# Kernel tuning notes

Measured on AMD Instinct MI355X. Metric: run time of the kernel, lower is better.

Reference implementation:

```python
import jax, jax.numpy as jnp
import numpy as np

N_NODES = 100000
N_EDGES = 1600000
DIMS = [64, 64, 64, 32]  # [n_feat] + hid


def setup_inputs() -> dict:
    key = jax.random.key(0)
    ks = jax.random.split(key, 2 + 2 * (len(DIMS) - 1))
    x = jax.random.normal(ks[0], (N_NODES, DIMS[0]), dtype=jnp.float32)
    edge_index = jax.random.randint(ks[1], (2, N_EDGES), 0, N_NODES, dtype=jnp.int64)
    inp = {"x": x, "edge_index": edge_index}
    for i in range(len(DIMS) - 1):
        fan_in, fan_out = DIMS[i], DIMS[i + 1]
        scale = 1.0 / np.sqrt(fan_in)
        inp[f"W{i+1}"] = jax.random.normal(ks[2 + 2 * i], (fan_in, fan_out), dtype=jnp.float32) * scale
        inp[f"b{i+1}"] = jax.random.normal(ks[3 + 2 * i], (fan_out,), dtype=jnp.float32) * scale
    return inp


def _gcn_conv(x, W, b, src, dst, dis):
    # h = X W ; out[i] = sum_{j->i} norm_ij * h[j] + dis[i]^2 * h[i] + b
    h = x @ W
    norm = dis[src] * dis[dst]                      # [E]
    agg = jax.ops.segment_sum(h[src] * norm[:, None], dst, num_segments=x.shape[0])
    agg = agg + h * (dis * dis)[:, None]            # self-loop contribution
    return agg + b


def reference(x, edge_index, W1, b1, W2, b2, W3, b3):
    src, dst = edge_index[0], edge_index[1]
    n = x.shape[0]
    # degree with self-loops (edge weight 1), symmetric normalization
    deg = jax.ops.segment_sum(jnp.ones(src.shape[0], x.dtype), dst, num_segments=n) + 1.0
    dis = jax.lax.rsqrt(deg)
    h = jax.nn.relu(_gcn_conv(x, W1, b1, src, dst, dis))   # dropout is identity in eval
    h = jax.nn.relu(_gcn_conv(h, W2, b2, src, dst, dis))
    return _gcn_conv(h, W3, b3, src, dst, dis)
```

## Files before the change

kernel.cpp:

```cpp
#include <hip/hip_runtime.h>


typedef __attribute__((ext_vector_type(8))) _Float16 half8;
typedef __attribute__((ext_vector_type(4))) _Float16 half4;

static inline int cdiv(int a, int b) { return (a + b - 1) / b; }

#define ACHUNK 8192
#define MAXNBK 512

__global__ void k_bucket_hist(const int* __restrict__ dst, int* __restrict__ counts_t,
                              int NBK, int NBA, int E) {
    __shared__ int cnt[MAXNBK];
    int t = threadIdx.x, b = blockIdx.x;
    for (int i = t; i < NBK; i += 256) cnt[i] = 0;
    __syncthreads();
    int e0 = b * ACHUNK;
#pragma unroll 8
    for (int j = 0; j < ACHUNK / 256; ++j) {
        int e = e0 + j * 256 + t;
        if (e < E) atomicAdd(&cnt[dst[e] >> 8], 1);
    }
    __syncthreads();
    for (int i = t; i < NBK; i += 256) counts_t[i * NBA + b] = cnt[i];
}

#define SCAN_T 256
#define SCAN_V 4
#define SCAN_CHUNK 1024

__global__ void k_scan_partial(const int* __restrict__ a, int* __restrict__ bsum, int n) {
    __shared__ int red[SCAN_T];
    int t = threadIdx.x, b = blockIdx.x;
    int base = b * SCAN_CHUNK + t * SCAN_V;
    int s = 0;
#pragma unroll
    for (int j = 0; j < SCAN_V; ++j) { int i = base + j; if (i < n) s += a[i]; }
    red[t] = s;
    __syncthreads();
    for (int off = SCAN_T / 2; off > 0; off >>= 1) {
        if (t < off) red[t] += red[t + off];
        __syncthreads();
    }
    if (t == 0) bsum[b] = red[0];
}

__global__ void k_scan_final(const int* __restrict__ a, const int* __restrict__ bsum,
                             int* __restrict__ out, int nb, int n) {
    __shared__ int sb[256];
    __shared__ int sh[SCAN_T];
    int t = threadIdx.x, bk = blockIdx.x;
    sb[t] = (t < nb) ? bsum[t] : 0;
    __syncthreads();
    for (int off = 1; off < 256; off <<= 1) {
        int u = (t >= off) ? sb[t - off] : 0;
        __syncthreads();
        sb[t] += u;
        __syncthreads();
    }
    int bbase = (bk == 0) ? 0 : sb[bk - 1];
    int base = bk * SCAN_CHUNK + t * SCAN_V;
    int v[SCAN_V];
    int s = 0;
#pragma unroll
    for (int j = 0; j < SCAN_V; ++j) {
        int i = base + j;
        v[j] = (i < n) ? a[i] : 0;
        s += v[j];
    }
    sh[t] = s;
    __syncthreads();
    for (int off = 1; off < SCAN_T; off <<= 1) {
        int u = (t >= off) ? sh[t - off] : 0;
        __syncthreads();
        sh[t] += u;
        __syncthreads();
    }
    int run = sh[t] - s + bbase;
#pragma unroll
    for (int j = 0; j < SCAN_V; ++j) {
        int i = base + j;
        if (i < n) { out[i] = run; run += v[j]; }
    }
}

__global__ void k_bucket_scatter(const int* __restrict__ src, const int* __restrict__ dst,
                                 const int* __restrict__ offsets, unsigned* __restrict__ bucketed,
                                 int NBK, int NBA, int E) {
    __shared__ int curs[MAXNBK];
    int t = threadIdx.x, b = blockIdx.x;
    for (int i = t; i < NBK; i += 256) curs[i] = offsets[i * NBA + b];
    __syncthreads();
    int e0 = b * ACHUNK;
#pragma unroll 8
    for (int j = 0; j < ACHUNK / 256; ++j) {
        int e = e0 + j * 256 + t;
        if (e < E) {
            int d = dst[e];
            int pos = atomicAdd(&curs[d >> 8], 1);
            bucketed[pos] = (unsigned)src[e] | ((unsigned)(d & 255) << 24);
        }
    }
}

__global__ void k_bucket_build(const unsigned* __restrict__ bucketed,
                               const int* __restrict__ offsets,
                               int* __restrict__ csr_src, int* __restrict__ row_start,
                               float* __restrict__ dis, int NBK, int NBA, int N, int E) {
    __shared__ int cnt[256];
    __shared__ int sc[256];
    int t = threadIdx.x, k = blockIdx.x;
    int base = offsets[k * NBA];
    int end = (k + 1 < NBK) ? offsets[(k + 1) * NBA] : E;
    cnt[t] = 0;
    __syncthreads();
    for (int i = base + t; i < end; i += 256)
        atomicAdd(&cnt[bucketed[i] >> 24], 1);
    __syncthreads();
    int c = cnt[t];
    sc[t] = c;
    __syncthreads();
    for (int off = 1; off < 256; off <<= 1) {
        int u = (t >= off) ? sc[t - off] : 0;
        __syncthreads();
        sc[t] += u;
        __syncthreads();
    }
    int excl = sc[t] - c;
    int node = k * 256 + t;
    if (node < N) {
        row_start[node] = base + excl;
        dis[node] = rsqrtf(1.0f + (float)c);
    }
    if (k == 0 && t == 0) row_start[N] = E;
    cnt[t] = base + excl;
    __syncthreads();
    for (int i = base + t; i < end; i += 256) {
        unsigned w = bucketed[i];
        int pos = atomicAdd(&cnt[w >> 24], 1);
        csr_src[pos] = (int)(w & 0xFFFFFFu);
    }
}

template <int K, int M>
__global__ void k_gemm_f(const float* __restrict__ X, const float* __restrict__ W,
                         const float* __restrict__ dis, _Float16* __restrict__ H, int n) {
    constexpr int TPR = M / 8;
    constexpr int ROWS = 256 / TPR;
    constexpr int KP = K + 1;
    __shared__ float Ws[K * M];
    __shared__ float Xs[ROWS * KP];
    int tid = threadIdx.x;
    for (int idx = tid; idx < K * M / 4; idx += 256)
        ((float4*)Ws)[idx] = ((const float4*)W)[idx];
    int row0 = blockIdx.x * ROWS;
    for (int idx = tid; idx < ROWS * (K / 4); idx += 256) {
        int r = idx / (K / 4), kq = idx % (K / 4);
        int row = row0 + r;
        float4 vv = (row < n) ? ((const float4*)X)[(size_t)row * (K / 4) + kq]
                              : make_float4(0.f, 0.f, 0.f, 0.f);
        Xs[r * KP + kq * 4 + 0] = vv.x;
        Xs[r * KP + kq * 4 + 1] = vv.y;
        Xs[r * KP + kq * 4 + 2] = vv.z;
        Xs[r * KP + kq * 4 + 3] = vv.w;
    }
    __syncthreads();
    int r = tid / TPR, c0 = (tid % TPR) * 8;
    int row = row0 + r;
    if (row >= n) return;
    float4 a0 = make_float4(0.f, 0.f, 0.f, 0.f);
    float4 a1 = make_float4(0.f, 0.f, 0.f, 0.f);
#pragma unroll
    for (int k = 0; k < K; ++k) {
        float xv = Xs[r * KP + k];
        float4 w0 = ((const float4*)Ws)[(k * M + c0) / 4];
        float4 w1 = ((const float4*)Ws)[(k * M + c0) / 4 + 1];
        a0.x = fmaf(xv, w0.x, a0.x);
        a0.y = fmaf(xv, w0.y, a0.y);
        a0.z = fmaf(xv, w0.z, a0.z);
        a0.w = fmaf(xv, w0.w, a0.w);
        a1.x = fmaf(xv, w1.x, a1.x);
        a1.y = fmaf(xv, w1.y, a1.y);
        a1.z = fmaf(xv, w1.z, a1.z);
        a1.w = fmaf(xv, w1.w, a1.w);
    }
    float dn = dis[row];
    half8 hv;
    hv[0] = (_Float16)(a0.x * dn);
    hv[1] = (_Float16)(a0.y * dn);
    hv[2] = (_Float16)(a0.z * dn);
    hv[3] = (_Float16)(a0.w * dn);
    hv[4] = (_Float16)(a1.x * dn);
    hv[5] = (_Float16)(a1.y * dn);
    hv[6] = (_Float16)(a1.z * dn);
    hv[7] = (_Float16)(a1.w * dn);
    ((half8*)H)[(size_t)row * (M / 8) + c0 / 8] = hv;
}

template <int MOUT>
__global__ __launch_bounds__(256, 8)
void k_fused_agg_gemm(const _Float16* __restrict__ h, const float* __restrict__ dis,
                      const int* __restrict__ row_start, const int* __restrict__ csr_src,
                      const float* __restrict__ bagg, const float* __restrict__ W,
                      _Float16* __restrict__ H, int n) {
    constexpr int K = 64, KP = K + 1;
    __shared__ __align__(16) _Float16 Ws[K * MOUT];
    __shared__ float Xs[32 * KP];
    int tid = threadIdx.x;
    for (int idx = tid; idx < K * MOUT / 4; idx += 256) {
        float4 wv = ((const float4*)W)[idx];
        half4 h4;
        h4[0] = (_Float16)wv.x;
        h4[1] = (_Float16)wv.y;
        h4[2] = (_Float16)wv.z;
        h4[3] = (_Float16)wv.w;
        ((half4*)Ws)[idx] = h4;
    }

    int wave = tid >> 6, lane = tid & 63;
    int sub = lane >> 3, fl = lane & 7;
    int node0 = blockIdx.x * 32;
    int node = node0 + wave * 8 + sub;
    if (node < n) {
        const half8* h8 = (const half8*)h;
        float acc[8];
#pragma unroll
        for (int j = 0; j < 8; ++j) acc[j] = 0.f;
        int e = row_start[node], e1 = row_start[node + 1];
        for (; e + 7 < e1; e += 8) {
            int s0 = csr_src[e], s1 = csr_src[e + 1];
            int s2 = csr_src[e + 2], s3 = csr_src[e + 3];
            int s4 = csr_src[e + 4], s5 = csr_src[e + 5];
            int s6 = csr_src[e + 6], s7 = csr_src[e + 7];
            half8 v0 = h8[(size_t)s0 * 8 + fl];
            half8 v1 = h8[(size_t)s1 * 8 + fl];
            half8 v2 = h8[(size_t)s2 * 8 + fl];
            half8 v3 = h8[(size_t)s3 * 8 + fl];
            half8 v4 = h8[(size_t)s4 * 8 + fl];
            half8 v5 = h8[(size_t)s5 * 8 + fl];
            half8 v6 = h8[(size_t)s6 * 8 + fl];
            half8 v7 = h8[(size_t)s7 * 8 + fl];
#pragma unroll
            for (int j = 0; j < 8; ++j)
                acc[j] += (((float)v0[j] + (float)v1[j]) + ((float)v2[j] + (float)v3[j])) +
                          (((float)v4[j] + (float)v5[j]) + ((float)v6[j] + (float)v7[j]));
        }
        for (; e + 3 < e1; e += 4) {
            int s0 = csr_src[e], s1 = csr_src[e + 1];
            int s2 = csr_src[e + 2], s3 = csr_src[e + 3];
            half8 v0 = h8[(size_t)s0 * 8 + fl];
            half8 v1 = h8[(size_t)s1 * 8 + fl];
            half8 v2 = h8[(size_t)s2 * 8 + fl];
            half8 v3 = h8[(size_t)s3 * 8 + fl];
#pragma unroll
            for (int j = 0; j < 8; ++j)
                acc[j] += ((float)v0[j] + (float)v1[j]) + ((float)v2[j] + (float)v3[j]);
        }
        for (; e < e1; ++e) {
            int s0 = csr_src[e];
            half8 v0 = h8[(size_t)s0 * 8 + fl];
#pragma unroll
            for (int j = 0; j < 8; ++j) acc[j] += (float)v0[j];
        }
        float dn = dis[node];
        half8 hv = h8[(size_t)node * 8 + fl];
        float4 b0 = ((const float4*)bagg)[fl * 2];
        float4 b1 = ((const float4*)bagg)[fl * 2 + 1];
        int rrow = wave * 8 + sub;
        float* xp = &Xs[rrow * KP + fl * 8];
        xp[0] = fmaxf((acc[0] + (float)hv[0]) * dn + b0.x, 0.f);
        xp[1] = fmaxf((acc[1] + (float)hv[1]) * dn + b0.y, 0.f);
        xp[2] = fmaxf((acc[2] + (float)hv[2]) * dn + b0.z, 0.f);
        xp[3] = fmaxf((acc[3] + (float)hv[3]) * dn + b0.w, 0.f);
        xp[4] = fmaxf((acc[4] + (float)hv[4]) * dn + b1.x, 0.f);
        xp[5] = fmaxf((acc[5] + (float)hv[5]) * dn + b1.y, 0.f);
        xp[6] = fmaxf((acc[6] + (float)hv[6]) * dn + b1.z, 0.f);
        xp[7] = fmaxf((acc[7] + (float)hv[7]) * dn + b1.w, 0.f);
    }
    __syncthreads();

    constexpr int TPR = MOUT / 8;
    int r = tid / TPR, c0 = (tid % TPR) * 8;
    int row = node0 + r;
    if (r >= 32 || row >= n) return;
    float4 a0 = make_float4(0.f, 0.f, 0.f, 0.f);
    float4 a1 = make_float4(0.f, 0.f, 0.f, 0.f);
#pragma unroll
    for (int k = 0; k < K; ++k) {
        float xv = Xs[r * KP + k];
        half8 w = ((const half8*)Ws)[(k * MOUT + c0) / 8];
        a0.x = fmaf(xv, (float)w[0], a0.x);
        a0.y = fmaf(xv, (float)w[1], a0.y);
        a0.z = fmaf(xv, (float)w[2], a0.z);
        a0.w = fmaf(xv, (float)w[3], a0.w);
        a1.x = fmaf(xv, (float)w[4], a1.x);
        a1.y = fmaf(xv, (float)w[5], a1.y);
        a1.z = fmaf(xv, (float)w[6], a1.z);
        a1.w = fmaf(xv, (float)w[7], a1.w);
    }
    float dn = dis[row];
    half8 hv;
    hv[0] = (_Float16)(a0.x * dn);
    hv[1] = (_Float16)(a0.y * dn);
    hv[2] = (_Float16)(a0.z * dn);
    hv[3] = (_Float16)(a0.w * dn);
    hv[4] = (_Float16)(a1.x * dn);
    hv[5] = (_Float16)(a1.y * dn);
    hv[6] = (_Float16)(a1.z * dn);
    hv[7] = (_Float16)(a1.w * dn);
    ((half8*)H)[(size_t)row * (MOUT / 8) + c0 / 8] = hv;
}

__global__ __launch_bounds__(256, 8)
void k_aggregate32(const _Float16* __restrict__ h, const float* __restrict__ dis,
                   const int* __restrict__ row_start, const int* __restrict__ csr_src,
                   const float* __restrict__ b, float* __restrict__ out, int n) {
    constexpr int LPN = 4, NPW = 16;
    int gtid = blockIdx.x * blockDim.x + threadIdx.x;
    int wave = gtid >> 6;
    int lane = threadIdx.x & 63;
    int sub = lane / LPN, fl = lane % LPN;
    int node = wave * NPW + sub;
    if (node >= n) return;
    const half8* h8 = (const half8*)h;
    float acc[8];
#pragma unroll
    for (int j = 0; j < 8; ++j) acc[j] = 0.f;
    int e = row_start[node], e1 = row_start[node + 1];
    for (; e + 7 < e1; e += 8) {
        int s0 = csr_src[e], s1 = csr_src[e + 1];
        int s2 = csr_src[e + 2], s3 = csr_src[e + 3];
        int s4 = csr_src[e + 4], s5 = csr_src[e + 5];
        int s6 = csr_src[e + 6], s7 = csr_src[e + 7];
        half8 v0 = h8[(size_t)s0 * LPN + fl];
        half8 v1 = h8[(size_t)s1 * LPN + fl];
        half8 v2 = h8[(size_t)s2 * LPN + fl];
        half8 v3 = h8[(size_t)s3 * LPN + fl];
        half8 v4 = h8[(size_t)s4 * LPN + fl];
        half8 v5 = h8[(size_t)s5 * LPN + fl];
        half8 v6 = h8[(size_t)s6 * LPN + fl];
        half8 v7 = h8[(size_t)s7 * LPN + fl];
#pragma unroll
        for (int j = 0; j < 8; ++j)
            acc[j] += (((float)v0[j] + (float)v1[j]) + ((float)v2[j] + (float)v3[j])) +
                      (((float)v4[j] + (float)v5[j]) + ((float)v6[j] + (float)v7[j]));
    }
    for (; e + 3 < e1; e += 4) {
        int s0 = csr_src[e], s1 = csr_src[e + 1];
        int s2 = csr_src[e + 2], s3 = csr_src[e + 3];
        half8 v0 = h8[(size_t)s0 * LPN + fl];
        half8 v1 = h8[(size_t)s1 * LPN + fl];
        half8 v2 = h8[(size_t)s2 * LPN + fl];
        half8 v3 = h8[(size_t)s3 * LPN + fl];
#pragma unroll
        for (int j = 0; j < 8; ++j)
            acc[j] += ((float)v0[j] + (float)v1[j]) + ((float)v2[j] + (float)v3[j]);
    }
    for (; e < e1; ++e) {
        int s0 = csr_src[e];
        half8 v0 = h8[(size_t)s0 * LPN + fl];
#pragma unroll
        for (int j = 0; j < 8; ++j) acc[j] += (float)v0[j];
    }
    float dn = dis[node];
    half8 hv = h8[(size_t)node * LPN + fl];
    float4 b0 = ((const float4*)b)[fl * 2];
    float4 b1 = ((const float4*)b)[fl * 2 + 1];
    float4* op = (float4*)(out + ((size_t)node * LPN + fl) * 8);
    op[0] = make_float4((acc[0] + (float)hv[0]) * dn + b0.x,
                        (acc[1] + (float)hv[1]) * dn + b0.y,
                        (acc[2] + (float)hv[2]) * dn + b0.z,
                        (acc[3] + (float)hv[3]) * dn + b0.w);
    op[1] = make_float4((acc[4] + (float)hv[4]) * dn + b1.x,
                        (acc[5] + (float)hv[5]) * dn + b1.y,
                        (acc[6] + (float)hv[6]) * dn + b1.z,
                        (acc[7] + (float)hv[7]) * dn + b1.w);
}

extern "C" void kernel_launch(void* const* d_in, const int* in_sizes, int n_in,
                              void* d_out, int out_size, void* d_ws, size_t ws_size,
                              hipStream_t stream) {
    const float* x   = (const float*)d_in[0];
    const int*   ei  = (const int*)d_in[1];
    const float* W1  = (const float*)d_in[2];
    const float* b1  = (const float*)d_in[3];
    const float* W2  = (const float*)d_in[4];
    const float* b2  = (const float*)d_in[5];
    const float* W3  = (const float*)d_in[6];
    const float* b3  = (const float*)d_in[7];
    float* out = (float*)d_out;

    const int N = in_sizes[0] / 64;
    const int E = in_sizes[1] / 2;
    const int* src = ei;
    const int* dst = ei + E;

    const int NBK = cdiv(N, 256);
    const int NBA = cdiv(E, ACHUNK);
    const int nmat = NBK * NBA;

    const size_t Np = (size_t)((N + 63) / 64) * 64;
    char* p = (char*)d_ws;
    int*      counts_t = (int*)p;      p += (size_t)nmat * sizeof(int);
    int*      offsets  = (int*)p;      p += (size_t)nmat * sizeof(int);
    int*      bsum     = (int*)p;      p += 1024 * sizeof(int);
    int*      row_start= (int*)p;      p += (Np + 64) * sizeof(int);
    float*    dis      = (float*)p;    p += Np * sizeof(float);
    unsigned* bucketed = (unsigned*)p; p += (size_t)E * sizeof(unsigned);
    int*      csr_src  = (int*)p;      p += (size_t)E * sizeof(int);
    _Float16* bufA     = (_Float16*)p; p += Np * 64 * sizeof(_Float16);
    _Float16* bufB     = (_Float16*)p; p += Np * 64 * sizeof(_Float16);
    (void)ws_size;

    const int B = 256;
    const int nb = cdiv(nmat, SCAN_CHUNK);

    k_bucket_hist<<<NBA, B, 0, stream>>>(dst, counts_t, NBK, NBA, E);
    k_scan_partial<<<nb, B, 0, stream>>>(counts_t, bsum, nmat);
    k_scan_final<<<nb, B, 0, stream>>>(counts_t, bsum, offsets, nb, nmat);
    k_bucket_scatter<<<NBA, B, 0, stream>>>(src, dst, offsets, bucketed, NBK, NBA, E);
    k_bucket_build<<<NBK, B, 0, stream>>>(bucketed, offsets, csr_src, row_start, dis,
                                          NBK, NBA, N, E);

    k_gemm_f<64, 64><<<cdiv(N, 32), B, 0, stream>>>(x, W1, dis, bufA, N);
    k_fused_agg_gemm<64><<<cdiv(N, 32), B, 0, stream>>>(
        bufA, dis, row_start, csr_src, b1, W2, bufB, N);
    k_fused_agg_gemm<32><<<cdiv(N, 32), B, 0, stream>>>(
        bufB, dis, row_start, csr_src, b2, W3, bufA, N);
    k_aggregate32<<<cdiv(cdiv(N, 16) * 64, B), B, 0, stream>>>(
        bufA, dis, row_start, csr_src, b3, out, N);
}
```

Measured before the change: 302.2 us.

## Stage bucket scatter and CSR build in LDS, add nontemporal index loads

The bucket scatter kernel now sorts each chunk locally in shared memory by bucket key and writes contiguous runs to global memory, replacing scattered per-edge global writes. The chunk size is halved so the staging buffers fit in shared memory. The CSR build kernel also sorts each bucket in shared memory before a coalesced write when the bucket fits. Edge-index and csr_src loads use nontemporal hints, and the fused aggregate+GEMM uses 8 threads per row with variable columns per thread. The extra LDS use lowers occupancy, and the added scan and sync steps add overhead.

New measurement: 297.7 us. No clear change (-1.5%).

```diff
diff --git a/kernel.cpp b/kernel.cpp
--- a/kernel.cpp
+++ b/kernel.cpp
@@ -6,7 +6,7 @@
 
 static inline int cdiv(int a, int b) { return (a + b - 1) / b; }
 
-#define ACHUNK 8192
+#define ACHUNK 4096
 #define MAXNBK 512
 
 __global__ void k_bucket_hist(const int* __restrict__ dst, int* __restrict__ counts_t,
@@ -19,7 +19,10 @@
 #pragma unroll 8
     for (int j = 0; j < ACHUNK / 256; ++j) {
         int e = e0 + j * 256 + t;
-        if (e < E) atomicAdd(&cnt[dst[e] >> 8], 1);
+        if (e < E) {
+            int d = __builtin_nontemporal_load(dst + e);
+            atomicAdd(&cnt[d >> 8], 1);
+        }
     }
     __syncthreads();
     for (int i = t; i < NBK; i += 256) counts_t[i * NBA + b] = cnt[i];
@@ -84,31 +87,72 @@
     }
 }
 
-__global__ void k_bucket_scatter(const int* __restrict__ src, const int* __restrict__ dst,
-                                 const int* __restrict__ offsets, unsigned* __restrict__ bucketed,
-                                 int NBK, int NBA, int E) {
-    __shared__ int curs[MAXNBK];
+__global__ __launch_bounds__(256)
+void k_bucket_scatter(const int* __restrict__ src, const int* __restrict__ dst,
+                      const int* __restrict__ offsets, unsigned* __restrict__ bucketed,
+                      int NBK, int NBA, int E) {
+    __shared__ unsigned w_s[ACHUNK];
+    __shared__ unsigned o_s[ACHUNK];
+    __shared__ unsigned short k_s[ACHUNK];
+    __shared__ unsigned short ksort[ACHUNK];
+    __shared__ int cnt[512];
+    __shared__ int exs[512];
     int t = threadIdx.x, b = blockIdx.x;
-    for (int i = t; i < NBK; i += 256) curs[i] = offsets[i * NBA + b];
-    __syncthreads();
     int e0 = b * ACHUNK;
-#pragma unroll 8
+    int m = E - e0; if (m > ACHUNK) m = ACHUNK;
+    cnt[t] = 0; cnt[t + 256] = 0;
+#pragma unroll
     for (int j = 0; j < ACHUNK / 256; ++j) {
-        int e = e0 + j * 256 + t;
-        if (e < E) {
-            int d = dst[e];
-            int pos = atomicAdd(&curs[d >> 8], 1);
-            bucketed[pos] = (unsigned)src[e] | ((unsigned)(d & 255) << 24);
-        }
-    }
-}
-
+        int idx = j * 256 + t;
+        if (idx < m) {
+            int e = e0 + idx;
+            int s = __builtin_nontemporal_load(src + e);
+            int d = __builtin_nontemporal_load(dst + e);
+            w_s[idx] = (unsigned)s | ((unsigned)(d & 255) << 24);
+            k_s[idx] = (unsigned short)(d >> 8);
+        }
+    }
+    __syncthreads();
+    for (int idx = t; idx < m; idx += 256) atomicAdd(&cnt[k_s[idx]], 1);
+    __syncthreads();
+    exs[t] = cnt[t]; exs[t + 256] = cnt[t + 256];
+    __syncthreads();
+    for (int off = 1; off < 512; off <<= 1) {
+        int v0 = (t >= off) ? exs[t - off] : 0;
+        int v1 = (t + 256 >= off) ? exs[t + 256 - off] : 0;
+        __syncthreads();
+        exs[t] += v0; exs[t + 256] += v1;
+        __syncthreads();
+    }
+    int excl0 = exs[t] - cnt[t];
+    int excl1 = exs[t + 256] - cnt[t + 256];
+    __syncthreads();
+    cnt[t] = excl0;
+    cnt[t + 256] = excl1;
+    if (t < NBK)       exs[t]       = offsets[t * NBA + b] - excl0;
+    if (t + 256 < NBK) exs[t + 256] = offsets[(t + 256) * NBA + b] - excl1;
+    __syncthreads();
+    for (int idx = t; idx < m; idx += 256) {
+        int k = k_s[idx];
+        int r = atomicAdd(&cnt[k], 1);
+        o_s[r] = w_s[idx];
+        ksort[r] = (unsigned short)k;
+    }
+    __syncthreads();
+    for (int idx = t; idx < m; idx += 256) {
+        int k = ksort[idx];
+        bucketed[exs[k] + idx] = o_s[idx];
+    }
+}
+
+#define BCAP 6144
 __global__ void k_bucket_build(const unsigned* __restrict__ bucketed,
                                const int* __restrict__ offsets,
                                int* __restrict__ csr_src, int* __restrict__ row_start,
                                float* __restrict__ dis, int NBK, int NBA, int N, int E) {
     __shared__ int cnt[256];
     __shared__ int sc[256];
+    __shared__ int srt[BCAP];
     int t = threadIdx.x, k = blockIdx.x;
     int base = offsets[k * NBA];
     int end = (k + 1 < NBK) ? offsets[(k + 1) * NBA] : E;
@@ -133,12 +177,24 @@
         dis[node] = rsqrtf(1.0f + (float)c);
     }
     if (k == 0 && t == 0) row_start[N] = E;
-    cnt[t] = base + excl;
-    __syncthreads();
-    for (int i = base + t; i < end; i += 256) {
-        unsigned w = bucketed[i];
-        int pos = atomicAdd(&cnt[w >> 24], 1);
-        csr_src[pos] = (int)(w & 0xFFFFFFu);
+    cnt[t] = excl;
+    __syncthreads();
+    int m = end - base;
+    if (m <= BCAP) {
+        for (int i = base + t; i < end; i += 256) {
+            unsigned w = bucketed[i];
+            int r = atomicAdd(&cnt[w >> 24], 1);
+            srt[r] = (int)(w & 0xFFFFFFu);
+        }
+        __syncthreads();
+        for (int idx = t; idx < m; idx += 256)
+            csr_src[base + idx] = srt[idx];
+    } else {
+        for (int i = base + t; i < end; i += 256) {
+            unsigned w = bucketed[i];
+            int pos = base + atomicAdd(&cnt[w >> 24], 1);
+            csr_src[pos] = (int)(w & 0xFFFFFFu);
+        }
     }
 }
 
@@ -228,10 +284,14 @@
         for (int j = 0; j < 8; ++j) acc[j] = 0.f;
         int e = row_start[node], e1 = row_start[node + 1];
         for (; e + 7 < e1; e += 8) {
-            int s0 = csr_src[e], s1 = csr_src[e + 1];
-            int s2 = csr_src[e + 2], s3 = csr_src[e + 3];
-            int s4 = csr_src[e + 4], s5 = csr_src[e + 5];
-            int s6 = csr_src[e + 6], s7 = csr_src[e + 7];
+            int s0 = __builtin_nontemporal_load(csr_src + e);
+            int s1 = __builtin_nontemporal_load(csr_src + e + 1);
+            int s2 = __builtin_nontemporal_load(csr_src + e + 2);
+            int s3 = __builtin_nontemporal_load(csr_src + e + 3);
+            int s4 = __builtin_nontemporal_load(csr_src + e + 4);
+            int s5 = __builtin_nontemporal_load(csr_src + e + 5);
+            int s6 = __builtin_nontemporal_load(csr_src + e + 6);
+            int s7 = __builtin_nontemporal_load(csr_src + e + 7);
             half8 v0 = h8[(size_t)s0 * 8 + fl];
             half8 v1 = h8[(size_t)s1 * 8 + fl];
             half8 v2 = h8[(size_t)s2 * 8 + fl];
@@ -246,8 +306,10 @@
                           (((float)v4[j] + (float)v5[j]) + ((float)v6[j] + (float)v7[j]));
         }
         for (; e + 3 < e1; e += 4) {
-            int s0 = csr_src[e], s1 = csr_src[e + 1];
-            int s2 = csr_src[e + 2], s3 = csr_src[e + 3];
+            int s0 = __builtin_nontemporal_load(csr_src + e);
+            int s1 = __builtin_nontemporal_load(csr_src + e + 1);
+            int s2 = __builtin_nontemporal_load(csr_src + e + 2);
+            int s3 = __builtin_nontemporal_load(csr_src + e + 3);
             half8 v0 = h8[(size_t)s0 * 8 + fl];
             half8 v1 = h8[(size_t)s1 * 8 + fl];
             half8 v2 = h8[(size_t)s2 * 8 + fl];
@@ -257,7 +319,7 @@
                 acc[j] += ((float)v0[j] + (float)v1[j]) + ((float)v2[j] + (float)v3[j]);
         }
         for (; e < e1; ++e) {
-            int s0 = csr_src[e];
+            int s0 = __builtin_nontemporal_load(csr_src + e);
             half8 v0 = h8[(size_t)s0 * 8 + fl];
 #pragma unroll
             for (int j = 0; j < 8; ++j) acc[j] += (float)v0[j];
@@ -279,36 +341,54 @@
     }
     __syncthreads();
 
-    constexpr int TPR = MOUT / 8;
-    int r = tid / TPR, c0 = (tid % TPR) * 8;
+    constexpr int TPR = 8;
+    constexpr int CPT = MOUT / TPR;
+    int r = tid / TPR, c0 = (tid % TPR) * CPT;
     int row = node0 + r;
-    if (r >= 32 || row >= n) return;
+    if (row >= n) return;
     float4 a0 = make_float4(0.f, 0.f, 0.f, 0.f);
     float4 a1 = make_float4(0.f, 0.f, 0.f, 0.f);
 #pragma unroll
     for (int k = 0; k < K; ++k) {
         float xv = Xs[r * KP + k];
-        half8 w = ((const half8*)Ws)[(k * MOUT + c0) / 8];
-        a0.x = fmaf(xv, (float)w[0], a0.x);
-        a0.y = fmaf(xv, (float)w[1], a0.y);
-        a0.z = fmaf(xv, (float)w[2], a0.z);
-        a0.w = fmaf(xv, (float)w[3], a0.w);
-        a1.x = fmaf(xv, (float)w[4], a1.x);
-        a1.y = fmaf(xv, (float)w[5], a1.y);
-        a1.z = fmaf(xv, (float)w[6], a1.z);
-        a1.w = fmaf(xv, (float)w[7], a1.w);
+        if constexpr (CPT == 8) {
+            half8 w = ((const half8*)Ws)[(k * MOUT + c0) / 8];
+            a0.x = fmaf(xv, (float)w[0], a0.x);
+            a0.y = fmaf(xv, (float)w[1], a0.y);
+            a0.z = fmaf(xv, (float)w[2], a0.z);
+            a0.w = fmaf(xv, (float)w[3], a0.w);
+            a1.x = fmaf(xv, (float)w[4], a1.x);
+            a1.y = fmaf(xv, (float)w[5], a1.y);
+            a1.z = fmaf(xv, (float)w[6], a1.z);
+            a1.w = fmaf(xv, (float)w[7], a1.w);
+        } else {
+            half4 w = ((const half4*)Ws)[(k * MOUT + c0) / 4];
+            a0.x = fmaf(xv, (float)w[0], a0.x);
+            a0.y = fmaf(xv, (float)w[1], a0.y);
+            a0.z = fmaf(xv, (float)w[2], a0.z);
+            a0.w = fmaf(xv, (float)w[3], a0.w);
+        }
     }
     float dn = dis[row];
-    half8 hv;
-    hv[0] = (_Float16)(a0.x * dn);
-    hv[1] = (_Float16)(a0.y * dn);
-    hv[2] = (_Float16)(a0.z * dn);
-    hv[3] = (_Float16)(a0.w * dn);
-    hv[4] = (_Float16)(a1.x * dn);
-    hv[5] = (_Float16)(a1.y * dn);
-    hv[6] = (_Float16)(a1.z * dn);
-    hv[7] = (_Float16)(a1.w * dn);
-    ((half8*)H)[(size_t)row * (MOUT / 8) + c0 / 8] = hv;
+    if constexpr (CPT == 8) {
+        half8 hv;
+        hv[0] = (_Float16)(a0.x * dn);
+        hv[1] = (_Float16)(a0.y * dn);
+        hv[2] = (_Float16)(a0.z * dn);
+        hv[3] = (_Float16)(a0.w * dn);
+        hv[4] = (_Float16)(a1.x * dn);
+        hv[5] = (_Float16)(a1.y * dn);
+        hv[6] = (_Float16)(a1.z * dn);
+        hv[7] = (_Float16)(a1.w * dn);
+        ((half8*)H)[(size_t)row * (MOUT / 8) + c0 / 8] = hv;
+    } else {
+        half4 hv;
+        hv[0] = (_Float16)(a0.x * dn);
+        hv[1] = (_Float16)(a0.y * dn);
+        hv[2] = (_Float16)(a0.z * dn);
+        hv[3] = (_Float16)(a0.w * dn);
+        ((half4*)H)[(size_t)row * (MOUT / 4) + c0 / 4] = hv;
+    }
 }
 
 __global__ __launch_bounds__(256, 8)
@@ -328,10 +408,14 @@
     for (int j = 0; j < 8; ++j) acc[j] = 0.f;
     int e = row_start[node], e1 = row_start[node + 1];
     for (; e + 7 < e1; e += 8) {
-        int s0 = csr_src[e], s1 = csr_src[e + 1];
-        int s2 = csr_src[e + 2], s3 = csr_src[e + 3];
-        int s4 = csr_src[e + 4], s5 = csr_src[e + 5];
-        int s6 = csr_src[e + 6], s7 = csr_src[e + 7];
+        int s0 = __builtin_nontemporal_load(csr_src + e);
+        int s1 = __builtin_nontemporal_load(csr_src + e + 1);
+        int s2 = __builtin_nontemporal_load(csr_src + e + 2);
+        int s3 = __builtin_nontemporal_load(csr_src + e + 3);
+        int s4 = __builtin_nontemporal_load(csr_src + e + 4);
+        int s5 = __builtin_nontemporal_load(csr_src + e + 5);
+        int s6 = __builtin_nontemporal_load(csr_src + e + 6);
+        int s7 = __builtin_nontemporal_load(csr_src + e + 7);
         half8 v0 = h8[(size_t)s0 * LPN + fl];
         half8 v1 = h8[(size_t)s1 * LPN + fl];
         half8 v2 = h8[(size_t)s2 * LPN + fl];
@@ -346,8 +430,10 @@
                       (((float)v4[j] + (float)v5[j]) + ((float)v6[j] + (float)v7[j]));
     }
     for (; e + 3 < e1; e += 4) {
-        int s0 = csr_src[e], s1 = csr_src[e + 1];
-        int s2 = csr_src[e + 2], s3 = csr_src[e + 3];
+        int s0 = __builtin_nontemporal_load(csr_src + e);
+        int s1 = __builtin_nontemporal_load(csr_src + e + 1);
+        int s2 = __builtin_nontemporal_load(csr_src + e + 2);
+        int s3 = __builtin_nontemporal_load(csr_src + e + 3);
         half8 v0 = h8[(size_t)s0 * LPN + fl];
         half8 v1 = h8[(size_t)s1 * LPN + fl];
         half8 v2 = h8[(size_t)s2 * LPN + fl];
@@ -357,7 +443,7 @@
             acc[j] += ((float)v0[j] + (float)v1[j]) + ((float)v2[j] + (float)v3[j]);
     }
     for (; e < e1; ++e) {
-        int s0 = csr_src[e];
+        int s0 = __builtin_nontemporal_load(csr_src + e);
         half8 v0 = h8[(size_t)s0 * LPN + fl];
 #pragma unroll
         for (int j = 0; j < 8; ++j) acc[j] += (float)v0[j];
```
